# Optimization experiments

Measured on AMD Instinct MI355X. Metric: run time of the kernel, lower is better.

The kernel has to match this reference:

```python
import jax, jax.numpy as jnp
import numpy as np

D_MODEL = 256
D_HID = 128
EPS = 1e-5
MASK_VALUE = -10000.0


def _layer_norm(x, scale, bias):
    mu = jnp.mean(x, axis=-1, keepdims=True)
    var = jnp.mean(jnp.square(x - mu), axis=-1, keepdims=True)
    return (x - mu) * jax.lax.rsqrt(var + EPS) * scale + bias


def setup_inputs() -> dict:
    key = jax.random.key(0)
    ks = jax.random.split(key, 8)
    B, S = 32, 1024
    std = 0.02
    return {
        "x": jax.random.normal(ks[0], (B, S, D_MODEL), dtype=jnp.float32),
        "ln1_scale": jnp.ones((D_MODEL,), jnp.float32),
        "ln1_bias": jnp.zeros((D_MODEL,), jnp.float32),
        "w_qkv": jax.random.normal(ks[1], (D_MODEL, 3 * D_MODEL), jnp.float32) * std,
        "b_qkv": jnp.zeros((3 * D_MODEL,), jnp.float32),
        "w_proj": jax.random.normal(ks[2], (D_MODEL, D_MODEL), jnp.float32) * std,
        "b_proj": jnp.zeros((D_MODEL,), jnp.float32),
        "ln2_scale": jnp.ones((D_MODEL,), jnp.float32),
        "ln2_bias": jnp.zeros((D_MODEL,), jnp.float32),
        "w_fc1": jax.random.normal(ks[3], (D_MODEL, D_HID), jnp.float32) * std,
        "b_fc1": jnp.zeros((D_HID,), jnp.float32),
        "w_fc2": jax.random.normal(ks[4], (D_HID, D_MODEL), jnp.float32) * std,
        "b_fc2": jnp.zeros((D_MODEL,), jnp.float32),
    }


def reference(x, ln1_scale, ln1_bias, w_qkv, b_qkv, w_proj, b_proj,
              ln2_scale, ln2_bias, w_fc1, b_fc1, w_fc2, b_fc2):
    B, S, D = x.shape
    # --- pre-LN self-attention ---
    residual = x
    h = _layer_norm(x, ln1_scale, ln1_bias)
    qkv = h @ w_qkv + b_qkv                       # [B, S, 3D]
    q, k, v = jnp.split(qkv, 3, axis=2)           # each [B, S, D]; 1 head, head_dim=D
    scale = 1.0 / jnp.sqrt(jnp.asarray(D, x.dtype))
    scores = jnp.einsum('bqd,bkd->bqk', q, k) * scale   # [B, S, S]
    causal = jnp.tril(jnp.ones((S, S), dtype=bool))
    scores = jnp.where(causal[None, :, :], scores, MASK_VALUE)
    attn = jax.nn.softmax(scores, axis=-1)        # dropout is identity (eval mode)
    out = jnp.einsum('bqk,bkd->bqd', attn, v)     # [B, S, D]
    out = out @ w_proj + b_proj
    x = out + residual
    # --- pre-LN MLP ---
    residual = x
    h = _layer_norm(x, ln2_scale, ln2_bias)
    h = jax.nn.relu(h @ w_fc1 + b_fc1)
    h = h @ w_fc2 + b_fc2
    return h + residual
```

## Files before the change

### kernel.cpp

```cpp
#include <hip/hip_runtime.h>
#include <hip/hip_bf16.h>

#define D_MODEL 256
#define D_HID   128
#define SEQ     1024
#define NBATCH  32
#define NROWS   (NBATCH * SEQ)
#define MASKV   -10000.0f
#define EPSLN   1e-5f

typedef unsigned short u16;
using bf16x8 = __attribute__((ext_vector_type(8))) short;
using f32x4  = __attribute__((ext_vector_type(4))) float;

union U8 { uint4 v; u16 s[8]; };

__device__ __forceinline__ float bf2f(u16 u) {
    unsigned int x = ((unsigned int)u) << 16;
    return __uint_as_float(x);
}
__device__ __forceinline__ u16 f2bf(float f) {
    unsigned int u = __float_as_uint(f);
    u += 0x7fff + ((u >> 16) & 1);
    return (u16)(u >> 16);
}
__device__ __forceinline__ void load4(const float* p, float* f) {
    float4 a = *(const float4*)p;
    f[0] = a.x; f[1] = a.y; f[2] = a.z; f[3] = a.w;
}
__device__ __forceinline__ void load4(const u16* p, float* f) {
    ushort4 v = *(const ushort4*)p;
    f[0] = bf2f(v.x); f[1] = bf2f(v.y); f[2] = bf2f(v.z); f[3] = bf2f(v.w);
}
__device__ __forceinline__ void gload16(const u16* g, u16* l) {
    __builtin_amdgcn_global_load_lds(
        (const __attribute__((address_space(1))) void*)g,
        (__attribute__((address_space(3))) void*)l, 16, 0, 0);
}

template <int CTRL>
__device__ __forceinline__ float dpp_mov(float v) {
    return __int_as_float(__builtin_amdgcn_update_dpp(
        0, __float_as_int(v), CTRL, 0xf, 0xf, true));
}
__device__ __forceinline__ float red16_max(float v) {
    v = fmaxf(v, dpp_mov<0xB1>(v));
    v = fmaxf(v, dpp_mov<0x4E>(v));
    v = fmaxf(v, dpp_mov<0x141>(v));
    v = fmaxf(v, dpp_mov<0x140>(v));
    return v;
}
__device__ __forceinline__ float red16_sum(float v) {
    v += dpp_mov<0xB1>(v);
    v += dpp_mov<0x4E>(v);
    v += dpp_mov<0x141>(v);
    v += dpp_mov<0x140>(v);
    return v;
}

__global__ __launch_bounds__(256) void transpose_weights(
    const float* __restrict__ wqkv, u16* __restrict__ wqkvT,
    const float* __restrict__ wproj, u16* __restrict__ wprojT,
    const float* __restrict__ wfc1, u16* __restrict__ wfc1T,
    const float* __restrict__ wfc2, u16* __restrict__ wfc2T) {
    int tid = blockIdx.x * 256 + threadIdx.x;
    int stride = gridDim.x * 256;
    for (int i = tid; i < 768 * 256; i += stride) {
        int n = i >> 8, k = i & 255;
        wqkvT[i] = f2bf(wqkv[k * 768 + n]);
    }
    for (int i = tid; i < 256 * 256; i += stride) {
        int n = i >> 8, k = i & 255;
        wprojT[i] = f2bf(wproj[k * 256 + n]);
    }
    for (int i = tid; i < 128 * 256; i += stride) {
        int n = i >> 8, k = i & 255;
        wfc1T[i] = f2bf(wfc1[k * 128 + n]);
    }
    for (int i = tid; i < 256 * 128; i += stride) {
        int n = i >> 7, k = i & 127;
        wfc2T[i] = f2bf(wfc2[k * 256 + n]);
    }
}

template <typename TX>
__global__ __launch_bounds__(256) void ln_fused(
    const TX* __restrict__ x, const float* __restrict__ gamma,
    const float* __restrict__ beta, u16* __restrict__ out) {
    int wave = threadIdx.x >> 6, lane = threadIdx.x & 63;
    int row = blockIdx.x * 4 + wave;
    float f[4];
    load4(x + (size_t)row * D_MODEL + lane * 4, f);
    float s  = f[0] + f[1] + f[2] + f[3];
    float sq = f[0] * f[0] + f[1] * f[1] + f[2] * f[2] + f[3] * f[3];
    #pragma unroll
    for (int off = 1; off < 64; off <<= 1) {
        s  += __shfl_xor(s, off);
        sq += __shfl_xor(sq, off);
    }
    float mu   = s * (1.0f / 256.0f);
    float var  = sq * (1.0f / 256.0f) - mu * mu;
    float rstd = rsqrtf(var + EPSLN);
    float g[4], be[4];
    load4(gamma + lane * 4, g);
    load4(beta + lane * 4, be);
    ushort4 o;
    o.x = f2bf((f[0] - mu) * rstd * g[0] + be[0]);
    o.y = f2bf((f[1] - mu) * rstd * g[1] + be[1]);
    o.z = f2bf((f[2] - mu) * rstd * g[2] + be[2]);
    o.w = f2bf((f[3] - mu) * rstd * g[3] + be[3]);
    *(ushort4*)(out + (size_t)row * D_MODEL + lane * 4) = o;
}

#define GT2_ELEMS (2 * 128 * 128)

template <int K>
__device__ __forceinline__ void gemm_tile2(
    const u16* __restrict__ A, const u16* __restrict__ BT,
    int m0, int n0, u16* lds, f32x4 acc[4][4]) {
    u16* ldsA = lds;
    u16* ldsB = lds + 128 * 128;
    const int tid = threadIdx.x;
    const int lane = tid & 63, wave = tid >> 6;
    const int wr = (wave >> 1) * 64, wc = (wave & 1) * 64;
    const int row = lane & 15, quad = lane >> 4;

    for (int ks = 0; ks < K; ks += 128) {
        __syncthreads();
        #pragma unroll
        for (int i = 0; i < 8; i++) {
            int blk = i * 4 + wave;
            int B = (blk << 10) + lane * 16;
            int r = B >> 8;
            int cb = (B & 255) ^ ((r & 7) << 4);
            gload16(A + (size_t)(m0 + r) * K + ks + (cb >> 1),
                    ldsA + (blk << 9));
            gload16(BT + (size_t)(n0 + r) * K + ks + (cb >> 1),
                    ldsB + (blk << 9));
        }
        __syncthreads();
        #pragma unroll
        for (int k0 = 0; k0 < 128; k0 += 32) {
            bf16x8 a[4], b[4];
            #pragma unroll
            for (int mi = 0; mi < 4; mi++) {
                int rr = wr + mi * 16 + row;
                a[mi] = *(const bf16x8*)(ldsA + rr * 128 +
                         ((k0 + quad * 8) ^ ((rr & 7) << 3)));
            }
            #pragma unroll
            for (int nj = 0; nj < 4; nj++) {
                int rr = wc + nj * 16 + row;
                b[nj] = *(const bf16x8*)(ldsB + rr * 128 +
                         ((k0 + quad * 8) ^ ((rr & 7) << 3)));
            }
            #pragma unroll
            for (int mi = 0; mi < 4; mi++)
                #pragma unroll
                for (int nj = 0; nj < 4; nj++)
                    acc[mi][nj] = __builtin_amdgcn_mfma_f32_16x16x32_bf16(
                        a[mi], b[nj], acc[mi][nj], 0, 0, 0);
        }
    }
}

#define ZERO_ACC4(acc)                                       \
    _Pragma("unroll") for (int i_ = 0; i_ < 4; i_++)         \
    _Pragma("unroll") for (int j_ = 0; j_ < 4; j_++)         \
    _Pragma("unroll") for (int e_ = 0; e_ < 4; e_++) acc[i_][j_][e_] = 0.0f;

#define EPILOG_IDX4                                          \
    int lane = threadIdx.x & 63, wave = threadIdx.x >> 6;    \
    int wr = (wave >> 1) * 64, wc = (wave & 1) * 64;         \
    int row = lane & 15, quad = lane >> 4;

__global__ __launch_bounds__(256) void gemm_qkv(
    const u16* __restrict__ h, const u16* __restrict__ wqkvT,
    const float* __restrict__ b_qkv,
    u16* __restrict__ q, u16* __restrict__ kk, u16* __restrict__ vT) {
    __shared__ u16 lds[GT2_ELEMS];
    f32x4 acc[4][4];
    ZERO_ACC4(acc)
    int m0 = blockIdx.x * 128, n0 = blockIdx.y * 128;
    gemm_tile2<256>(h, wqkvT, m0, n0, lds, acc);
    EPILOG_IDX4
    #pragma unroll
    for (int mi = 0; mi < 4; mi++) {
        #pragma unroll
        for (int nj = 0; nj < 4; nj++) {
            int gn = n0 + wc + nj * 16 + row;
            float bias = b_qkv[gn];
            int gm = m0 + wr + mi * 16 + quad * 4;
            if (gn < 256) {
                #pragma unroll
                for (int r = 0; r < 4; r++)
                    q[(size_t)(gm + r) * 256 + gn] =
                        f2bf((acc[mi][nj][r] + bias) * 0.0625f);
            } else if (gn < 512) {
                int col = gn - 256;
                #pragma unroll
                for (int r = 0; r < 4; r++)
                    kk[(size_t)(gm + r) * 256 + col] = f2bf(acc[mi][nj][r] + bias);
            } else {
                int d = gn - 512;
                int b = gm >> 10, s = gm & 1023;
                ushort4 pack;
                pack.x = f2bf(acc[mi][nj][0] + bias);
                pack.y = f2bf(acc[mi][nj][1] + bias);
                pack.z = f2bf(acc[mi][nj][2] + bias);
                pack.w = f2bf(acc[mi][nj][3] + bias);
                *(ushort4*)(vT + ((size_t)(b * 256 + d) << 10) + s) = pack;
            }
        }
    }
}

__global__ __launch_bounds__(256) void gemm_proj(
    const u16* __restrict__ ao, const u16* __restrict__ wprojT,
    const float* __restrict__ b_proj, const float* __restrict__ x_in,
    u16* __restrict__ x2) {
    __shared__ u16 lds[GT2_ELEMS];
    f32x4 acc[4][4];
    ZERO_ACC4(acc)
    int m0 = blockIdx.x * 128, n0 = blockIdx.y * 128;
    gemm_tile2<256>(ao, wprojT, m0, n0, lds, acc);
    EPILOG_IDX4
    #pragma unroll
    for (int mi = 0; mi < 4; mi++)
        #pragma unroll
        for (int nj = 0; nj < 4; nj++) {
            int gn = n0 + wc + nj * 16 + row;
            float bias = b_proj[gn];
            int gm = m0 + wr + mi * 16 + quad * 4;
            #pragma unroll
            for (int r = 0; r < 4; r++) {
                size_t idx = (size_t)(gm + r) * 256 + gn;
                x2[idx] = f2bf(acc[mi][nj][r] + bias + x_in[idx]);
            }
        }
}

__global__ __launch_bounds__(256) void gemm_fc1(
    const u16* __restrict__ h2, const u16* __restrict__ wfc1T,
    const float* __restrict__ b_fc1, u16* __restrict__ a1) {
    __shared__ u16 lds[GT2_ELEMS];
    f32x4 acc[4][4];
    ZERO_ACC4(acc)
    int m0 = blockIdx.x * 128, n0 = 0;
    gemm_tile2<256>(h2, wfc1T, m0, n0, lds, acc);
    EPILOG_IDX4
    #pragma unroll
    for (int mi = 0; mi < 4; mi++)
        #pragma unroll
        for (int nj = 0; nj < 4; nj++) {
            int gn = wc + nj * 16 + row;
            float bias = b_fc1[gn];
            int gm = m0 + wr + mi * 16 + quad * 4;
            #pragma unroll
            for (int r = 0; r < 4; r++) {
                float v = acc[mi][nj][r] + bias;
                a1[(size_t)(gm + r) * 128 + gn] = f2bf(fmaxf(v, 0.0f));
            }
        }
}

__global__ __launch_bounds__(256) void gemm_fc2(
    const u16* __restrict__ a1, const u16* __restrict__ wfc2T,
    const float* __restrict__ b_fc2, const u16* __restrict__ x2,
    float* __restrict__ out) {
    __shared__ u16 lds[GT2_ELEMS];
    f32x4 acc[4][4];
    ZERO_ACC4(acc)
    int m0 = blockIdx.x * 128, n0 = blockIdx.y * 128;
    gemm_tile2<128>(a1, wfc2T, m0, n0, lds, acc);
    EPILOG_IDX4
    #pragma unroll
    for (int mi = 0; mi < 4; mi++)
        #pragma unroll
        for (int nj = 0; nj < 4; nj++) {
            int gn = n0 + wc + nj * 16 + row;
            float bias = b_fc2[gn];
            int gm = m0 + wr + mi * 16 + quad * 4;
            #pragma unroll
            for (int r = 0; r < 4; r++) {
                size_t idx = (size_t)(gm + r) * 256 + gn;
                out[idx] = acc[mi][nj][r] + bias + bf2f(x2[idx]);
            }
        }
}

__constant__ unsigned char WQT[24] = {7,15,15,14,14,6,13,13,12,12,5,11,
                                      11,10,10,4,9,9,8,8,3,2,1,0};
__constant__ unsigned char WH[24]  = {2,0,1,0,1,2,0,1,0,1,2,0,
                                      1,0,1,2,0,1,0,1,2,2,2,2};

__global__ __launch_bounds__(256) void attn_kernel(
    const u16* __restrict__ q, const u16* __restrict__ k,
    const u16* __restrict__ vT, u16* __restrict__ ao,
    u16* __restrict__ part, float* __restrict__ ml) {
    __shared__ u16 k_lds[2][32 * 256];
    __shared__ u16 v_lds[2][256 * 32];
    __shared__ u16 p_lds[4][16 * 40];

    int j = blockIdx.x;
    int b = j & 31, w = j >> 5;
    int qt = WQT[w], hh = WH[w];
    int lo, hi;
    if (hh == 2) { lo = 0; hi = 2 * qt + 2; }
    else         { lo = hh * (qt + 1); hi = lo + qt + 1; }

    int tid = threadIdx.x;
    int lane = tid & 63, wave = tid >> 6;
    int row = lane & 15, quad = lane >> 4;
    int q0 = qt * 64;
    int qrow0 = q0 + wave * 16;

    const u16* qb = q + ((size_t)b << 10) * 256;
    const u16* kb = k + ((size_t)b << 10) * 256;
    const u16* vb = vT + (((size_t)b * 256) << 10);

    const int kxor = (row & 7) << 3;
    const int vxor = (row & 6) << 2;

    bf16x8 qf[8];
    #pragma unroll
    for (int kf = 0; kf < 8; kf++)
        qf[kf] = *(const bf16x8*)(qb + (size_t)(qrow0 + row) * 256 + kf * 32 + quad * 8);

    f32x4 o[16];
    #pragma unroll
    for (int n = 0; n < 16; n++)
        #pragma unroll
        for (int e = 0; e < 4; e++) o[n][e] = 0.0f;
    float m_i[4], l_i[4];
    #pragma unroll
    for (int r = 0; r < 4; r++) { m_i[r] = -1e30f; l_i[r] = 0.0f; }

    int wlast = 2 * qt + (wave >> 1);

    auto stage = [&](int bf, int kt) {
        int k0 = kt << 5;
        #pragma unroll
        for (int c = 0; c < 4; c++) {
            int blk = wave * 4 + c;
            int B = (blk << 10) + lane * 16;
            int rk = B >> 9;
            int ck = (B & 511) ^ ((rk & 7) << 4);
            gload16(kb + (size_t)(k0 + rk) * 256 + (ck >> 1),
                    &k_lds[bf][blk << 9]);
            int rv = B >> 6;
            int cv = (B & 63) ^ ((rv & 6) << 3);
            gload16(vb + ((size_t)rv << 10) + k0 + (cv >> 1),
                    &v_lds[bf][blk << 9]);
        }
    };

    stage(0, lo);
    __syncthreads();

    for (int kt = lo; kt < hi; kt++) {
        int cur = (kt - lo) & 1;
        if (kt + 1 < hi) stage(cur ^ 1, kt + 1);
        if (kt <= wlast) {
            const u16* kl = k_lds[cur];
            const u16* vl = v_lds[cur];

            f32x4 sf[2];
            #pragma unroll
            for (int jn = 0; jn < 2; jn++)
                #pragma unroll
                for (int e = 0; e < 4; e++) sf[jn][e] = 0.0f;
            __builtin_amdgcn_s_setprio(1);
            #pragma unroll
            for (int kf = 0; kf < 8; kf++)
                #pragma unroll
                for (int jn = 0; jn < 2; jn++) {
                    bf16x8 bfrag = *(const bf16x8*)(kl +
                        ((((jn * 16 + row) * 256) + kf * 32 + quad * 8) ^ kxor));
                    sf[jn] = __builtin_amdgcn_mfma_f32_16x16x32_bf16(
                        qf[kf], bfrag, sf[jn], 0, 0, 0);
                }
            __builtin_amdgcn_s_setprio(0);

            int kk0 = kt * 32;
            bool diag = (kt == wlast);
            int qrow = qrow0 + quad * 4;
            float sv[2][4];
            #pragma unroll
            for (int jn = 0; jn < 2; jn++)
                #pragma unroll
                for (int r = 0; r < 4; r++) {
                    float v = sf[jn][r];
                    if (diag && (kk0 + jn * 16 + row > qrow + r)) v = MASKV;
                    sv[jn][r] = v;
                }

            float pmax[4];
            int need = 0;
            #pragma unroll
            for (int r = 0; r < 4; r++) {
                pmax[r] = red16_max(fmaxf(sv[0][r], sv[1][r]));
                need |= (pmax[r] > m_i[r] + 8.0f) ? 1 : 0;
            }
            if (__any(need)) {
                #pragma unroll
                for (int r = 0; r < 4; r++) {
                    float mnew = fmaxf(m_i[r], pmax[r]);
                    float al = __expf(m_i[r] - mnew);
                    m_i[r] = mnew;
                    l_i[r] *= al;
                    #pragma unroll
                    for (int n = 0; n < 16; n++) o[n][r] *= al;
                }
            }
            #pragma unroll
            for (int r = 0; r < 4; r++) {
                float ps = 0.0f;
                #pragma unroll
                for (int jn = 0; jn < 2; jn++) {
                    sv[jn][r] = __expf(sv[jn][r] - m_i[r]);
                    ps += sv[jn][r];
                }
                l_i[r] += red16_sum(ps);
            }

            u16* pw = p_lds[wave];
            #pragma unroll
            for (int jn = 0; jn < 2; jn++)
                #pragma unroll
                for (int r = 0; r < 4; r++)
                    pw[(quad * 4 + r) * 40 + jn * 16 + row] = f2bf(sv[jn][r]);
            bf16x8 pf = *(const bf16x8*)(pw + row * 40 + quad * 8);

            __builtin_amdgcn_s_setprio(1);
            #pragma unroll
            for (int n = 0; n < 16; n++) {
                bf16x8 bv = *(const bf16x8*)(vl +
                    ((((n * 16 + row) * 32) + quad * 8) ^ vxor));
                o[n] = __builtin_amdgcn_mfma_f32_16x16x32_bf16(pf, bv, o[n], 0, 0, 0);
            }
            __builtin_amdgcn_s_setprio(0);
        }
        __syncthreads();
    }

    if (hh == 2) {
        float inv[4];
        #pragma unroll
        for (int r = 0; r < 4; r++) inv[r] = 1.0f / l_i[r];
        u16* aob = ao + (((size_t)b << 10) + qrow0) * 256;
        #pragma unroll
        for (int r = 0; r < 4; r++)
            #pragma unroll
            for (int n = 0; n < 16; n++)
                aob[(size_t)(quad * 4 + r) * 256 + n * 16 + row] =
                    f2bf(o[n][r] * inv[r]);
    } else {
        int p = (((b << 3) | (qt - 8)) << 1) | hh;
        u16* pb = part + (((size_t)p) << 6) * 256;
        #pragma unroll
        for (int r = 0; r < 4; r++) {
            int rt = wave * 16 + quad * 4 + r;
            #pragma unroll
            for (int n = 0; n < 16; n++)
                pb[(size_t)rt * 256 + n * 16 + row] = f2bf(o[n][r]);
        }
        if (row == 0) {
            #pragma unroll
            for (int r = 0; r < 4; r++) {
                int rt = wave * 16 + quad * 4 + r;
                float2 v2; v2.x = m_i[r]; v2.y = l_i[r];
                *(float2*)(ml + ((size_t)((p << 6) + rt)) * 2) = v2;
            }
        }
    }
}

__global__ __launch_bounds__(256) void attn_merge(
    const u16* __restrict__ part, const float* __restrict__ ml,
    u16* __restrict__ ao) {
    int j = blockIdx.x;
    int b = j >> 3, qi = j & 7;
    int t = threadIdx.x;
    int r = t >> 2, cq = t & 3;
    int pA = j << 1, pB = pA | 1;
    const float* mlA = ml + ((size_t)(pA << 6) + r) * 2;
    const float* mlB = ml + ((size_t)(pB << 6) + r) * 2;
    float mA = mlA[0], lA = mlA[1];
    float mB = mlB[0], lB = mlB[1];
    float m  = fmaxf(mA, mB);
    float eA = __expf(mA - m), eB = __expf(mB - m);
    float inv = 1.0f / (lA * eA + lB * eB);
    float sA = eA * inv, sB = eB * inv;
    const u16* oA = part + (((size_t)(pA << 6) + r) * 256) + cq * 64;
    const u16* oB = part + (((size_t)(pB << 6) + r) * 256) + cq * 64;
    u16* dst = ao + ((size_t)((b << 10) + 512 + (qi << 6) + r)) * 256 + cq * 64;
    #pragma unroll
    for (int u = 0; u < 8; u++) {
        U8 a, bb, o;
        a.v  = *(const uint4*)(oA + u * 8);
        bb.v = *(const uint4*)(oB + u * 8);
        #pragma unroll
        for (int e = 0; e < 8; e++)
            o.s[e] = f2bf(bf2f(a.s[e]) * sA + bf2f(bb.s[e]) * sB);
        *(uint4*)(dst + u * 8) = o.v;
    }
}

extern "C" void kernel_launch(void* const* d_in, const int* in_sizes, int n_in,
                              void* d_out, int out_size, void* d_ws, size_t ws_size,
                              hipStream_t stream) {
    const float* x      = (const float*)d_in[0];
    const float* ln1_s  = (const float*)d_in[1];
    const float* ln1_b  = (const float*)d_in[2];
    const float* w_qkv  = (const float*)d_in[3];
    const float* b_qkv  = (const float*)d_in[4];
    const float* w_proj = (const float*)d_in[5];
    const float* b_proj = (const float*)d_in[6];
    const float* ln2_s  = (const float*)d_in[7];
    const float* ln2_b  = (const float*)d_in[8];
    const float* w_fc1  = (const float*)d_in[9];
    const float* b_fc1  = (const float*)d_in[10];
    const float* w_fc2  = (const float*)d_in[11];
    const float* b_fc2  = (const float*)d_in[12];
    float* out = (float*)d_out;

    u16* h  = (u16*)d_out;
    u16* h2 = h + (size_t)NROWS * 256;

    u16* W = (u16*)d_ws;
    u16* wqkvT  = W;
    u16* wprojT = wqkvT + 196608;
    u16* wfc1T  = wprojT + 65536;
    u16* wfc2T  = wfc1T + 32768;
    u16* buf1   = wfc2T + 32768;
    u16* buf2   = buf1 + (size_t)NROWS * 256;
    u16* buf3   = buf2 + (size_t)NROWS * 256;

    u16*   part  = h;
    float* mlbuf = (float*)h2;

    transpose_weights<<<dim3(64), dim3(256), 0, stream>>>(
        w_qkv, wqkvT, w_proj, wprojT, w_fc1, wfc1T, w_fc2, wfc2T);
    ln_fused<float><<<dim3(NROWS / 4), dim3(256), 0, stream>>>(
        x, ln1_s, ln1_b, h);
    gemm_qkv<<<dim3(NROWS / 128, 6), dim3(256), 0, stream>>>(
        h, wqkvT, b_qkv, buf1, buf2, buf3);
    attn_kernel<<<dim3(768), dim3(256), 0, stream>>>(
        buf1, buf2, buf3, buf1, part, mlbuf);
    attn_merge<<<dim3(256), dim3(256), 0, stream>>>(
        part, mlbuf, buf1);
    gemm_proj<<<dim3(NROWS / 128, 2), dim3(256), 0, stream>>>(
        buf1, wprojT, b_proj, x, buf2);
    ln_fused<u16><<<dim3(NROWS / 4), dim3(256), 0, stream>>>(
        buf2, ln2_s, ln2_b, h2);
    gemm_fc1<<<dim3(NROWS / 128, 1), dim3(256), 0, stream>>>(
        h2, wfc1T, b_fc1, buf3);
    gemm_fc2<<<dim3(NROWS / 128, 2), dim3(256), 0, stream>>>(
        buf3, wfc2T, b_fc2, buf2, out);
}
```

Baseline: 251.7 us.

## Fuse LN2, fc1 and fc2 into one MLP kernel; single-buffer V in attention

```diff
diff --git a/kernel.cpp b/kernel.cpp
--- a/kernel.cpp
+++ b/kernel.cpp
@@ -240,66 +240,189 @@
         }
 }
 
-__global__ __launch_bounds__(256) void gemm_fc1(
-    const u16* __restrict__ h2, const u16* __restrict__ wfc1T,
-    const float* __restrict__ b_fc1, u16* __restrict__ a1) {
-    __shared__ u16 lds[GT2_ELEMS];
-    f32x4 acc[4][4];
-    ZERO_ACC4(acc)
-    int m0 = blockIdx.x * 128, n0 = 0;
-    gemm_tile2<256>(h2, wfc1T, m0, n0, lds, acc);
-    EPILOG_IDX4
+__global__ __launch_bounds__(256) void gemm_mlp(
+    const u16* __restrict__ x2, const float* __restrict__ g2,
+    const float* __restrict__ be2,
+    const u16* __restrict__ wfc1T, const float* __restrict__ b_fc1,
+    const u16* __restrict__ wfc2T, const float* __restrict__ b_fc2,
+    float* __restrict__ out) {
+    __shared__ u16 lds[65536];
+    u16* ldsB1 = lds + 32768;
+    u16* ldsA1 = lds + 49152;
+    const int tid = threadIdx.x;
+    const int lane = tid & 63, wave = tid >> 6;
+    const int rowl = lane & 15, quad = lane >> 4;
+    const int wr = (wave >> 1) * 64, wc = (wave & 1) * 64;
+    const int m0 = blockIdx.x * 128;
+
+    #pragma unroll
+    for (int i = 0; i < 16; i++) {
+        int blk = i * 4 + wave;
+        int B = (blk << 10) + lane * 16;
+        int r = B >> 9;
+        int cb = (B & 511) ^ ((r & 7) << 4);
+        gload16(x2 + (size_t)(m0 + r) * 256 + (cb >> 1), lds + (B >> 1));
+    }
+    #pragma unroll
+    for (int i = 0; i < 8; i++) {
+        int blk = i * 4 + wave;
+        int B = (blk << 10) + lane * 16;
+        int r = B >> 8;
+        int cb = (B & 255) ^ ((r & 7) << 4);
+        gload16(wfc1T + (size_t)r * 256 + 0 + (cb >> 1), ldsB1 + (B >> 1));
+    }
+    __syncthreads();
+
+    {
+        float4 g4  = *(const float4*)(g2 + lane * 4);
+        float4 be4 = *(const float4*)(be2 + lane * 4);
+        #pragma unroll 4
+        for (int i = 0; i < 32; i++) {
+            int r = wave + i * 4;
+            char* p = (char*)lds + r * 512 + ((lane * 8) ^ ((r & 7) << 4));
+            ushort4 v = *(ushort4*)p;
+            float f0 = bf2f(v.x), f1 = bf2f(v.y), f2v = bf2f(v.z), f3 = bf2f(v.w);
+            float s  = f0 + f1 + f2v + f3;
+            float sq = f0*f0 + f1*f1 + f2v*f2v + f3*f3;
+            s = red16_sum(s);   s += __shfl_xor(s, 16);   s += __shfl_xor(s, 32);
+            sq = red16_sum(sq); sq += __shfl_xor(sq, 16); sq += __shfl_xor(sq, 32);
+            float mu   = s * (1.0f / 256.0f);
+            float var  = sq * (1.0f / 256.0f) - mu * mu;
+            float rstd = rsqrtf(var + EPSLN);
+            ushort4 o;
+            o.x = f2bf((f0  - mu) * rstd * g4.x + be4.x);
+            o.y = f2bf((f1  - mu) * rstd * g4.y + be4.y);
+            o.z = f2bf((f2v - mu) * rstd * g4.z + be4.z);
+            o.w = f2bf((f3  - mu) * rstd * g4.w + be4.w);
+            *(ushort4*)p = o;
+        }
+    }
+    __syncthreads();
+
+    f32x4 acc1[4][4];
+    ZERO_ACC4(acc1)
+    #pragma unroll
+    for (int ks = 0; ks < 256; ks += 128) {
+        if (ks) {
+            __syncthreads();
+            #pragma unroll
+            for (int i = 0; i < 8; i++) {
+                int blk = i * 4 + wave;
+                int B = (blk << 10) + lane * 16;
+                int r = B >> 8;
+                int cb = (B & 255) ^ ((r & 7) << 4);
+                gload16(wfc1T + (size_t)r * 256 + ks + (cb >> 1),
+                        ldsB1 + (B >> 1));
+            }
+            __syncthreads();
+        }
+        #pragma unroll
+        for (int k0 = 0; k0 < 128; k0 += 32) {
+            bf16x8 a[4], b[4];
+            #pragma unroll
+            for (int mi = 0; mi < 4; mi++) {
+                int rr = wr + mi * 16 + rowl;
+                a[mi] = *(const bf16x8*)((const char*)lds + rr * 512 +
+                         ((((ks + k0 + quad * 8) << 1)) ^ ((rr & 7) << 4)));
+            }
+            #pragma unroll
+            for (int nj = 0; nj < 4; nj++) {
+                int rb = wc + nj * 16 + rowl;
+                b[nj] = *(const bf16x8*)((const char*)ldsB1 + rb * 256 +
+                         ((((k0 + quad * 8) << 1)) ^ ((rb & 7) << 4)));
+            }
+            #pragma unroll
+            for (int mi = 0; mi < 4; mi++)
+                #pragma unroll
+                for (int nj = 0; nj < 4; nj++)
+                    acc1[mi][nj] = __builtin_amdgcn_mfma_f32_16x16x32_bf16(
+                        a[mi], b[nj], acc1[mi][nj], 0, 0, 0);
+        }
+    }
     #pragma unroll
     for (int mi = 0; mi < 4; mi++)
         #pragma unroll
         for (int nj = 0; nj < 4; nj++) {
-            int gn = wc + nj * 16 + row;
-            float bias = b_fc1[gn];
-            int gm = m0 + wr + mi * 16 + quad * 4;
+            int gn_l = wc + nj * 16 + rowl;
+            float bias = b_fc1[gn_l];
             #pragma unroll
             for (int r = 0; r < 4; r++) {
-                float v = acc[mi][nj][r] + bias;
-                a1[(size_t)(gm + r) * 128 + gn] = f2bf(fmaxf(v, 0.0f));
-            }
-        }
-}
-
-__global__ __launch_bounds__(256) void gemm_fc2(
-    const u16* __restrict__ a1, const u16* __restrict__ wfc2T,
-    const float* __restrict__ b_fc2, const u16* __restrict__ x2,
-    float* __restrict__ out) {
-    __shared__ u16 lds[GT2_ELEMS];
-    f32x4 acc[4][4];
-    ZERO_ACC4(acc)
-    int m0 = blockIdx.x * 128, n0 = blockIdx.y * 128;
-    gemm_tile2<128>(a1, wfc2T, m0, n0, lds, acc);
-    EPILOG_IDX4
+                int gm_l = wr + mi * 16 + quad * 4 + r;
+                *(u16*)((char*)ldsA1 + gm_l * 256 +
+                        (((gn_l << 1)) ^ ((gm_l & 7) << 4))) =
+                    f2bf(fmaxf(acc1[mi][nj][r] + bias, 0.0f));
+            }
+        }
+    __syncthreads();
+
+    #pragma unroll
+    for (int i = 0; i < 16; i++) {
+        int blk = i * 4 + wave;
+        int B = (blk << 10) + lane * 16;
+        int r = B >> 8;
+        int cb = (B & 255) ^ ((r & 7) << 4);
+        gload16(wfc2T + (size_t)r * 128 + (cb >> 1), lds + (B >> 1));
+    }
+    __syncthreads();
+
+    const int wc2 = (wave & 1) * 128;
+    f32x4 acc2[4][8];
     #pragma unroll
     for (int mi = 0; mi < 4; mi++)
         #pragma unroll
-        for (int nj = 0; nj < 4; nj++) {
-            int gn = n0 + wc + nj * 16 + row;
+        for (int nj = 0; nj < 8; nj++)
+            #pragma unroll
+            for (int e = 0; e < 4; e++) acc2[mi][nj][e] = 0.0f;
+    #pragma unroll
+    for (int k0 = 0; k0 < 128; k0 += 32) {
+        bf16x8 a[4], b[8];
+        #pragma unroll
+        for (int mi = 0; mi < 4; mi++) {
+            int rr = wr + mi * 16 + rowl;
+            a[mi] = *(const bf16x8*)((const char*)ldsA1 + rr * 256 +
+                     ((((k0 + quad * 8) << 1)) ^ ((rr & 7) << 4)));
+        }
+        #pragma unroll
+        for (int nj = 0; nj < 8; nj++) {
+            int rb = wc2 + nj * 16 + rowl;
+            b[nj] = *(const bf16x8*)((const char*)lds + rb * 256 +
+                     ((((k0 + quad * 8) << 1)) ^ ((rb & 7) << 4)));
+        }
+        #pragma unroll
+        for (int mi = 0; mi < 4; mi++)
+            #pragma unroll
+            for (int nj = 0; nj < 8; nj++)
+                acc2[mi][nj] = __builtin_amdgcn_mfma_f32_16x16x32_bf16(
+                    a[mi], b[nj], acc2[mi][nj], 0, 0, 0);
+    }
+    #pragma unroll
+    for (int mi = 0; mi < 4; mi++)
+        #pragma unroll
+        for (int nj = 0; nj < 8; nj++) {
+            int gn = wc2 + nj * 16 + rowl;
             float bias = b_fc2[gn];
             int gm = m0 + wr + mi * 16 + quad * 4;
             #pragma unroll
             for (int r = 0; r < 4; r++) {
                 size_t idx = (size_t)(gm + r) * 256 + gn;
-                out[idx] = acc[mi][nj][r] + bias + bf2f(x2[idx]);
-            }
-        }
-}
-
-__constant__ unsigned char WQT[24] = {7,15,15,14,14,6,13,13,12,12,5,11,
-                                      11,10,10,4,9,9,8,8,3,2,1,0};
-__constant__ unsigned char WH[24]  = {2,0,1,0,1,2,0,1,0,1,2,0,
-                                      1,0,1,2,0,1,0,1,2,2,2,2};
+                out[idx] = acc2[mi][nj][r] + bias + bf2f(x2[idx]);
+            }
+        }
+}
+
+__constant__ unsigned char WQT[24] = {7,15,15,14,14,6,13,13,
+                                      4,10,10,5,11,11,12,12,
+                                      9,0,1,2,3,9,8,8};
+__constant__ unsigned char WH[24]  = {2,0,1,0,1,2,0,1,
+                                      2,0,1,2,0,1,0,1,
+                                      0,2,2,2,2,1,0,1};
 
 __global__ __launch_bounds__(256) void attn_kernel(
     const u16* __restrict__ q, const u16* __restrict__ k,
     const u16* __restrict__ vT, u16* __restrict__ ao,
     u16* __restrict__ part, float* __restrict__ ml) {
     __shared__ u16 k_lds[2][32 * 256];
-    __shared__ u16 v_lds[2][256 * 32];
+    __shared__ u16 v_lds[256 * 32];
     __shared__ u16 p_lds[4][16 * 40];
 
     int j = blockIdx.x;
@@ -338,7 +461,7 @@
 
     int wlast = 2 * qt + (wave >> 1);
 
-    auto stage = [&](int bf, int kt) {
+    auto stageK = [&](int bf, int kt) {
         int k0 = kt << 5;
         #pragma unroll
         for (int c = 0; c < 4; c++) {
@@ -348,22 +471,31 @@
             int ck = (B & 511) ^ ((rk & 7) << 4);
             gload16(kb + (size_t)(k0 + rk) * 256 + (ck >> 1),
                     &k_lds[bf][blk << 9]);
+        }
+    };
+    auto stageV = [&](int kt) {
+        int k0 = kt << 5;
+        #pragma unroll
+        for (int c = 0; c < 4; c++) {
+            int blk = wave * 4 + c;
+            int B = (blk << 10) + lane * 16;
             int rv = B >> 6;
             int cv = (B & 63) ^ ((rv & 6) << 3);
             gload16(vb + ((size_t)rv << 10) + k0 + (cv >> 1),
-                    &v_lds[bf][blk << 9]);
+                    &v_lds[blk << 9]);
         }
     };
 
-    stage(0, lo);
+    stageK(0, lo);
+    stageV(lo);
     __syncthreads();
 
     for (int kt = lo; kt < hi; kt++) {
         int cur = (kt - lo) & 1;
-        if (kt + 1 < hi) stage(cur ^ 1, kt + 1);
+        if (kt + 1 < hi) stageK(cur ^ 1, kt + 1);
         if (kt <= wlast) {
             const u16* kl = k_lds[cur];
-            const u16* vl = v_lds[cur];
+            const u16* vl = v_lds;
 
             f32x4 sf[2];
             #pragma unroll
@@ -441,6 +573,8 @@
             }
             __builtin_amdgcn_s_setprio(0);
         }
+        __syncthreads();
+        if (kt + 1 < hi) stageV(kt + 1);
         __syncthreads();
     }
 
@@ -552,10 +686,6 @@
         part, mlbuf, buf1);
     gemm_proj<<<dim3(NROWS / 128, 2), dim3(256), 0, stream>>>(
         buf1, wprojT, b_proj, x, buf2);
-    ln_fused<u16><<<dim3(NROWS / 4), dim3(256), 0, stream>>>(
-        buf2, ln2_s, ln2_b, h2);
-    gemm_fc1<<<dim3(NROWS / 128, 1), dim3(256), 0, stream>>>(
-        h2, wfc1T, b_fc1, buf3);
-    gemm_fc2<<<dim3(NROWS / 128, 2), dim3(256), 0, stream>>>(
-        buf3, wfc2T, b_fc2, buf2, out);
-}
+    gemm_mlp<<<dim3(NROWS / 128), dim3(256), 0, stream>>>(
+        buf2, ln2_s, ln2_b, wfc1T, b_fc1, wfc2T, b_fc2, out);
+}
```

New measurement: 250.8 us. Within noise of the previous version (-0.4%).
